# Kernel tuning notes

Measured on AMD Instinct MI355X. Metric: run time of the kernel, lower is better.

The kernel has to match this reference:

```python
import jax, jax.numpy as jnp
import numpy as np

NUM_EXPERTS = 8
TOP_K = 2
RANK = 16
LORA_ALPHA = 32
SCALING = LORA_ALPHA / RANK  # 2.0


def setup_inputs() -> dict:
    key = jax.random.key(0)
    ks = jax.random.split(key, 6)
    B, S, D_IN, D_OUT = 4, 2048, 4096, 4096
    x = jax.random.normal(ks[0], (B, S, D_IN), dtype=jnp.float32)
    W_base = jax.random.normal(ks[1], (D_OUT, D_IN), dtype=jnp.float32) * 0.02
    b_base = jax.random.normal(ks[2], (D_OUT,), dtype=jnp.float32) * 0.02
    W_router = jax.random.normal(ks[3], (NUM_EXPERTS, D_IN), dtype=jnp.float32) * 0.02
    A = jax.random.normal(ks[4], (NUM_EXPERTS, RANK, D_IN), dtype=jnp.float32) * 0.02
    Bm = jax.random.normal(ks[5], (D_OUT, RANK), dtype=jnp.float32) * 0.02
    Bm = jnp.broadcast_to(Bm, (NUM_EXPERTS, D_OUT, RANK)) * jnp.arange(1, NUM_EXPERTS + 1, dtype=jnp.float32)[:, None, None] * 0.2
    return {"x": x, "W_base": W_base, "b_base": b_base, "W_router": W_router, "A": A, "B": Bm}


def reference(x, W_base, b_base, W_router, A, B):
    bs, seq, d_in = x.shape
    T = bs * seq
    xf = x.reshape(T, d_in)  # flatten tokens, as in torch .view(-1, d_in)

    # base linear layer
    base = xf @ W_base.T + b_base  # [T, d_out]

    # local router: logits -> top-k -> softmax over selected weights
    logits = xf @ W_router.T                      # [T, E]
    rw, sel = jax.lax.top_k(logits, TOP_K)        # [T, K] each
    rw = jax.nn.softmax(rw, axis=-1)              # router_norm == 'softmax'

    # per-token per-expert combine weight (zero for unselected experts);
    # mathematically identical to gather-LoRA-scatter since top-k experts
    # per token are distinct.
    onehot = jax.nn.one_hot(sel, NUM_EXPERTS, dtype=rw.dtype)  # [T, K, E]
    w = jnp.einsum('tk,tke->te', rw, onehot)                   # [T, E]

    # LoRA: down-project to tiny rank, weight, then up-project; contract
    # expert+rank together to avoid a [T, E, d_out] intermediate.
    h = jnp.einsum('td,erd->ter', xf, A)          # [T, E, r] (small)
    lora = jnp.einsum('ter,te,eor->to', h, w, B) * SCALING  # [T, d_out]

    return (base + lora).reshape(bs, seq, -1)
```

## Files before the change

kernel.cpp:

```cpp
#include <hip/hip_runtime.h>
#include <hip/hip_bf16.h>
#include <stdint.h>

#define T_TOKENS 8192
#define DIN      4096
#define DOUT     4096
#define NE       8
#define RANK     16
#define KEXT     128
#define KTOT     4224
#define NT       66
#define SCALING  2.0f

typedef __attribute__((ext_vector_type(8))) short   short8;
typedef __attribute__((ext_vector_type(4))) float   float4v;

__device__ __forceinline__ unsigned short f2bf(float f) {
    union { float f; unsigned int u; } c; c.f = f;
    unsigned int u = c.u;
    u += 0x7FFFu + ((u >> 16) & 1u);
    return (unsigned short)(u >> 16);
}

#define GLD_LDS(g, l) __builtin_amdgcn_global_load_lds( \
    (const __attribute__((address_space(1))) void*)(g), \
    (__attribute__((address_space(3))) void*)(l), 16, 0, 0)

__global__ __launch_bounds__(256) void k_front(const float* __restrict__ x,
                                               const float* __restrict__ Wr,
                                               const float* __restrict__ Wb,
                                               const float* __restrict__ A,
                                               const float* __restrict__ Bm,
                                               unsigned short* __restrict__ xa,
                                               unsigned short* __restrict__ Wa,
                                               unsigned short* __restrict__ Acat,
                                               float* __restrict__ w8) {
    int b = blockIdx.x;
    int tid = threadIdx.x;

    if (b < 2048) {
        int l = tid & 63, w = tid >> 6;
        int t = b * 4 + w;
        const float4* x4 = (const float4*)x;
        const float4* Wr4 = (const float4*)Wr;
        unsigned short* xarow = xa + (size_t)t * KTOT;

        float racc[NE];
#pragma unroll
        for (int e = 0; e < NE; e++) racc[e] = 0.f;

#pragma unroll 4
        for (int ci = 0; ci < 16; ci++) {
            float4 xv = x4[(size_t)t * 1024 + ci * 64 + l];
            ushort4 p;
            p.x = f2bf(xv.x); p.y = f2bf(xv.y);
            p.z = f2bf(xv.z); p.w = f2bf(xv.w);
            *(ushort4*)(xarow + (ci * 64 + l) * 4) = p;
#pragma unroll
            for (int e = 0; e < NE; e++) {
                float4 wv = Wr4[e * 1024 + ci * 64 + l];
                racc[e] += xv.x * wv.x + xv.y * wv.y + xv.z * wv.z + xv.w * wv.w;
            }
        }
#pragma unroll
        for (int e = 0; e < NE; e++) {
            float v = racc[e];
#pragma unroll
            for (int off = 32; off > 0; off >>= 1) v += __shfl_xor(v, off);
            racc[e] = v;
        }
        if (l == 0) {
            int e0 = 0;
#pragma unroll
            for (int e = 1; e < NE; e++) if (racc[e] > racc[e0]) e0 = e;
            int e1 = -1;
#pragma unroll
            for (int e = 0; e < NE; e++)
                if (e != e0 && (e1 < 0 || racc[e] > racc[e1])) e1 = e;
            float a1 = __expf(racc[e1] - racc[e0]);
            float inv = 1.0f / (1.0f + a1);
            float* wrow = w8 + t * NE;
#pragma unroll
            for (int e = 0; e < NE; e++)
                wrow[e] = (e == e0) ? inv * SCALING : ((e == e1) ? a1 * inv * SCALING : 0.f);
        }
    } else if (b < 6144) {
        int base = (b - 2048) * 1024 + tid;
#pragma unroll
        for (int j = 0; j < 4; j++) {
            int idx = base + j * 256;
            float4 v = ((const float4*)Wb)[idx];
            int o  = idx >> 10;
            int kc = idx & 1023;
            ushort4 p;
            p.x = f2bf(v.x); p.y = f2bf(v.y); p.z = f2bf(v.z); p.w = f2bf(v.w);
            *(ushort4*)(Wa + (size_t)o * KTOT + kc * 4) = p;
        }
    } else {
        int idx = (b - 6144) * 256 + tid;
        if (idx < 131072) {
            float4 v = ((const float4*)A)[idx];
            ushort4 p;
            p.x = f2bf(v.x); p.y = f2bf(v.y); p.z = f2bf(v.z); p.w = f2bf(v.w);
            *(ushort4*)(Acat + (size_t)idx * 4) = p;
        } else {
            int j = idx - 131072;
            int o = j >> 5;
            int q = j & 31;
            int e = q >> 2;
            float4 v = ((const float4*)Bm)[(size_t)e * 16384 + o * 4 + (q & 3)];
            ushort4 p;
            p.x = f2bf(v.x); p.y = f2bf(v.y); p.z = f2bf(v.z); p.w = f2bf(v.w);
            *(ushort4*)(Wa + (size_t)o * KTOT + DIN + q * 4) = p;
        }
    }
}

#define STAGEH(kt, bb) do { \
    int k0_ = (kt) * 128; \
    _Pragma("unroll") \
    for (int it_ = 0; it_ < 2; it_++) { \
        int c_ = it_ * 256 + tid; \
        int row_ = c_ >> 4, s_ = c_ & 15; \
        int kc_ = s_ ^ (row_ & 15); \
        GLD_LDS(xa + (size_t)(m0 + row_) * KTOT + k0_ + kc_ * 8, lds_x + (bb) * 4096 + c_ * 8); \
    } \
    _Pragma("unroll") \
    for (int it_ = 0; it_ < 8; it_++) { \
        int c_ = it_ * 256 + tid; \
        int row_ = c_ >> 4, s_ = c_ & 15; \
        int kc_ = s_ ^ (row_ & 15); \
        GLD_LDS(Acat + (size_t)row_ * DIN + k0_ + kc_ * 8, lds_a + (bb) * 16384 + c_ * 8); \
    } \
} while (0)

__global__ __launch_bounds__(256) void k_h(unsigned short* __restrict__ xa,
                                           const unsigned short* __restrict__ Acat,
                                           const float* __restrict__ w8) {
    __shared__ unsigned short lds_x[2 * 32 * 128];
    __shared__ unsigned short lds_a[2 * 128 * 128];
    int m0  = blockIdx.x * 32;
    int tid = threadIdx.x;
    int l = tid & 63, w = tid >> 6;
    int quad = l >> 4, lr = l & 15;

    float4v acc[2][2] = {};

    STAGEH(0, 0);
    for (int kt = 0; kt < 32; ++kt) {
        int bb = kt & 1;
        if (kt + 1 < 32) {
            STAGEH(kt + 1, bb ^ 1);
            asm volatile("s_waitcnt vmcnt(10)" ::: "memory");
        } else {
            asm volatile("s_waitcnt vmcnt(0)" ::: "memory");
        }
        __syncthreads();
        const unsigned short* lx = lds_x + bb * 4096;
        const unsigned short* la = lds_a + bb * 16384;
#pragma unroll
        for (int kk = 0; kk < 4; kk++) {
            int kc = kk * 4 + quad;
            short8 a[2], bfr[2];
#pragma unroll
            for (int mi = 0; mi < 2; mi++) {
                int row = mi * 16 + lr;
                a[mi] = *(const short8*)&lx[row * 128 + ((kc ^ lr) * 8)];
            }
#pragma unroll
            for (int ni = 0; ni < 2; ni++) {
                int row = w * 32 + ni * 16 + lr;
                bfr[ni] = *(const short8*)&la[row * 128 + ((kc ^ lr) * 8)];
            }
#pragma unroll
            for (int mi = 0; mi < 2; mi++)
#pragma unroll
                for (int ni = 0; ni < 2; ni++)
                    acc[mi][ni] = __builtin_amdgcn_mfma_f32_16x16x32_bf16(a[mi], bfr[ni], acc[mi][ni], 0, 0, 0);
        }
        __syncthreads();
    }

#pragma unroll
    for (int mi = 0; mi < 2; mi++)
#pragma unroll
        for (int ni = 0; ni < 2; ni++) {
            int col = w * 32 + ni * 16 + lr;
            int e = col >> 4;
#pragma unroll
            for (int i = 0; i < 4; i++) {
                int t = m0 + mi * 16 + quad * 4 + i;
                float v = acc[mi][ni][i] * w8[t * NE + e];
                xa[(size_t)t * KTOT + DIN + col] = f2bf(v);
            }
        }
}

#define LOADA(dst, basep, mlo) { \
    _Pragma("unroll") for (int i_ = 0; i_ < 4; i_++) \
        dst[i_] = *(const short8*)((basep) + aoff + ((mlo) + i_) * 1024); }
#define LOADB(dst, basep) { \
    _Pragma("unroll") for (int i_ = 0; i_ < 4; i_++) \
        dst[i_] = *(const short8*)((basep) + boff + i_ * 1024); }
#define MFMA44(mlo) { \
    __builtin_amdgcn_s_setprio(1); \
    _Pragma("unroll") for (int i_ = 0; i_ < 4; i_++) \
    _Pragma("unroll") for (int j_ = 0; j_ < 4; j_++) \
        acc[(mlo) + i_][j_] = __builtin_amdgcn_mfma_f32_16x16x32_bf16(af[i_], bf[j_], acc[(mlo) + i_][j_], 0, 0, 0); \
    __builtin_amdgcn_s_setprio(0); }
#define STAGE(srcP, regbase, ts, kh, tb) do { \
    const unsigned short* s_ = (srcP) + (size_t)((ts) * 64 + (kh) * 32); \
    char* d_ = smem + (regbase) + (tb) * 32768 + (kh) * 16384 + tid16; \
    GLD_LDS(s_, d_); \
    GLD_LDS(s_ + (size_t)128 * KTOT, d_ + 8192); \
} while (0)
#define BAR() __builtin_amdgcn_s_barrier()
#define LGKM0() do { asm volatile("s_waitcnt lgkmcnt(0)" ::: "memory"); \
                     __builtin_amdgcn_sched_barrier(0); } while (0)

__global__ __launch_bounds__(512, 2) void k_main(const unsigned short* __restrict__ xa,
                                                 const unsigned short* __restrict__ Wa,
                                                 const float* __restrict__ bias,
                                                 float* __restrict__ out) {
    extern __shared__ char smem[];
    int tid = threadIdx.x;
    int l = tid & 63, w = tid >> 6;
    int lr = l & 15, quad = l >> 4;
    int wm = w >> 2, wn = w & 3;

    int bid = blockIdx.x;
    int xcd = bid & 7, idx = bid >> 3;
    int bm  = (xcd & 3) * 8 + (idx & 7);
    int bn  = (xcd >> 2) * 8 + (idx >> 3);

    int laneoff = (lr * 4 + (quad ^ ((lr >> 1) & 3))) * 16;
    int aoff = wm * 8192 + laneoff;
    int boff = wn * 4096 + laneoff;

    int srow  = w * 16 + ((tid >> 2) & 15);
    int skq   = (tid & 3) ^ ((tid >> 3) & 3);
    int tid16 = tid * 16;
    const unsigned short* srcA = xa + (size_t)(bm * 256 + srow) * KTOT + skq * 8;
    const unsigned short* srcB = Wa + (size_t)(bn * 256 + srow) * KTOT + skq * 8;

    float4v acc[8][4] = {};
    short8 af[4], bf[4];

    STAGE(srcA, 0,     0, 0, 0);
    STAGE(srcB, 65536, 0, 0, 0);
    STAGE(srcA, 0,     0, 1, 0);
    STAGE(srcB, 65536, 0, 1, 0);
    STAGE(srcA, 0,     1, 0, 1);
    STAGE(srcB, 65536, 1, 0, 1);
    asm volatile("s_waitcnt vmcnt(4)" ::: "memory");
    BAR();

    for (int t = 0; t < NT; ++t) {
        int buf  = t & 1, nbuf = buf ^ 1;
        int ts1  = (t + 1 < NT) ? t + 1 : NT - 1;
        int ts2  = (t + 2 < NT) ? t + 2 : NT - 1;
        const char* pa = smem + buf * 32768;
        const char* pb = smem + 65536 + buf * 32768;

        LOADA(af, pa, 0);
        LOADB(bf, pb);
        STAGE(srcA, 0, ts1, 1, nbuf);
        BAR(); LGKM0();
        MFMA44(0);
        BAR();

        LOADA(af, pa, 4);
        STAGE(srcB, 65536, ts1, 1, nbuf);
        BAR(); LGKM0();
        MFMA44(4);
        BAR();

        LOADA(af, pa + 16384, 0);
        LOADB(bf, pb + 16384);
        STAGE(srcA, 0, ts2, 0, buf);
        BAR(); LGKM0();
        MFMA44(0);
        BAR();

        LOADA(af, pa + 16384, 4);
        STAGE(srcB, 65536, ts2, 0, buf);
        asm volatile("s_waitcnt vmcnt(4)" ::: "memory");
        BAR(); LGKM0();
        MFMA44(4);
        BAR();
    }
    asm volatile("s_waitcnt vmcnt(0)" ::: "memory");

    int trow0 = bm * 256 + wm * 128;
    int ocol0 = bn * 256 + wn * 64;
#pragma unroll
    for (int ni = 0; ni < 4; ni++) {
        int o = ocol0 + ni * 16 + lr;
        float bb = bias[o];
#pragma unroll
        for (int mi = 0; mi < 8; mi++) {
#pragma unroll
            for (int i = 0; i < 4; i++) {
                int trow = trow0 + mi * 16 + quad * 4 + i;
                out[(size_t)trow * DOUT + o] = acc[mi][ni][i] + bb;
            }
        }
    }
}

extern "C" void kernel_launch(void* const* d_in, const int* in_sizes, int n_in,
                              void* d_out, int out_size, void* d_ws, size_t ws_size,
                              hipStream_t stream) {
    const float* x  = (const float*)d_in[0];
    const float* Wb = (const float*)d_in[1];
    const float* bb = (const float*)d_in[2];
    const float* Wr = (const float*)d_in[3];
    const float* A  = (const float*)d_in[4];
    const float* Bm = (const float*)d_in[5];
    float* out = (float*)d_out;

    char* ws = (char*)d_ws;
    unsigned short* xa   = (unsigned short*)(ws);
    unsigned short* Wa   = (unsigned short*)(ws + 69206016);
    unsigned short* Acat = (unsigned short*)(ws + 69206016 + 34603008);
    float*          w8   = (float*)(ws + 69206016 + 34603008 + 1048576);

    static bool attr_done = false;
    if (!attr_done) {
        hipFuncSetAttribute((const void*)k_main,
                            hipFuncAttributeMaxDynamicSharedMemorySize, 131072);
        attr_done = true;
    }

    k_front<<<dim3(7168),  dim3(256), 0, stream>>>(x, Wr, Wb, A, Bm, xa, Wa, Acat, w8);
    k_h    <<<dim3(256),   dim3(256), 0, stream>>>(xa, Acat, w8);
    k_main <<<dim3(512),   dim3(512), 131072, stream>>>(xa, Wa, bb, out);
}
```

Measured before the change: 590.0 us.

## Double-buffer LDS fragment registers to overlap ds_reads with MFMA

```diff
diff --git a/kernel.cpp b/kernel.cpp
--- a/kernel.cpp
+++ b/kernel.cpp
@@ -196,17 +196,17 @@
         }
 }
 
-#define LOADA(dst, basep, mlo) { \
+#define LOADA4(dst, basep, mlo) { \
     _Pragma("unroll") for (int i_ = 0; i_ < 4; i_++) \
         dst[i_] = *(const short8*)((basep) + aoff + ((mlo) + i_) * 1024); }
-#define LOADB(dst, basep) { \
+#define LOADB4(dst, basep) { \
     _Pragma("unroll") for (int i_ = 0; i_ < 4; i_++) \
         dst[i_] = *(const short8*)((basep) + boff + i_ * 1024); }
-#define MFMA44(mlo) { \
+#define MFMA44V(A_, B_, mlo) { \
     __builtin_amdgcn_s_setprio(1); \
     _Pragma("unroll") for (int i_ = 0; i_ < 4; i_++) \
     _Pragma("unroll") for (int j_ = 0; j_ < 4; j_++) \
-        acc[(mlo) + i_][j_] = __builtin_amdgcn_mfma_f32_16x16x32_bf16(af[i_], bf[j_], acc[(mlo) + i_][j_], 0, 0, 0); \
+        acc[(mlo) + i_][j_] = __builtin_amdgcn_mfma_f32_16x16x32_bf16(A_[i_], B_[j_], acc[(mlo) + i_][j_], 0, 0, 0); \
     __builtin_amdgcn_s_setprio(0); }
 #define STAGE(srcP, regbase, ts, kh, tb) do { \
     const unsigned short* s_ = (srcP) + (size_t)((ts) * 64 + (kh) * 32); \
@@ -215,8 +215,8 @@
     GLD_LDS(s_ + (size_t)128 * KTOT, d_ + 8192); \
 } while (0)
 #define BAR() __builtin_amdgcn_s_barrier()
-#define LGKM0() do { asm volatile("s_waitcnt lgkmcnt(0)" ::: "memory"); \
-                     __builtin_amdgcn_sched_barrier(0); } while (0)
+#define LGKMC(n) do { asm volatile("s_waitcnt lgkmcnt(" #n ")" ::: "memory"); \
+                      __builtin_amdgcn_sched_barrier(0); } while (0)
 
 __global__ __launch_bounds__(512, 2) void k_main(const unsigned short* __restrict__ xa,
                                                  const unsigned short* __restrict__ Wa,
@@ -244,7 +244,7 @@
     const unsigned short* srcB = Wa + (size_t)(bn * 256 + srow) * KTOT + skq * 8;
 
     float4v acc[8][4] = {};
-    short8 af[4], bf[4];
+    short8 afA[4], afB[4], bfA[4], bfB[4];
 
     STAGE(srcA, 0,     0, 0, 0);
     STAGE(srcB, 65536, 0, 0, 0);
@@ -254,42 +254,47 @@
     STAGE(srcB, 65536, 1, 0, 1);
     asm volatile("s_waitcnt vmcnt(4)" ::: "memory");
     BAR();
+    LOADA4(afA, smem, 0);
+    LOADB4(bfA, smem + 65536);
 
     for (int t = 0; t < NT; ++t) {
         int buf  = t & 1, nbuf = buf ^ 1;
         int ts1  = (t + 1 < NT) ? t + 1 : NT - 1;
         int ts2  = (t + 2 < NT) ? t + 2 : NT - 1;
-        const char* pa = smem + buf * 32768;
-        const char* pb = smem + 65536 + buf * 32768;
-
-        LOADA(af, pa, 0);
-        LOADB(bf, pb);
+        const char* pa  = smem + buf * 32768;
+        const char* pb  = smem + 65536 + buf * 32768;
+        const char* pan = smem + nbuf * 32768;
+        const char* pbn = smem + 65536 + nbuf * 32768;
+
+        LOADA4(afB, pa, 4);
         STAGE(srcA, 0, ts1, 1, nbuf);
-        BAR(); LGKM0();
-        MFMA44(0);
-        BAR();
-
-        LOADA(af, pa, 4);
+        BAR(); LGKMC(4);
+        MFMA44V(afA, bfA, 0);
+        BAR();
+
+        LOADA4(afA, pa + 16384, 0);
+        LOADB4(bfB, pb + 16384);
         STAGE(srcB, 65536, ts1, 1, nbuf);
-        BAR(); LGKM0();
-        MFMA44(4);
-        BAR();
-
-        LOADA(af, pa + 16384, 0);
-        LOADB(bf, pb + 16384);
+        BAR(); LGKMC(8);
+        MFMA44V(afB, bfA, 4);
+        BAR();
+
+        LOADA4(afB, pa + 16384, 4);
         STAGE(srcA, 0, ts2, 0, buf);
-        BAR(); LGKM0();
-        MFMA44(0);
-        BAR();
-
-        LOADA(af, pa + 16384, 4);
+        BAR(); LGKMC(4);
+        MFMA44V(afA, bfB, 0);
+        BAR();
+
         STAGE(srcB, 65536, ts2, 0, buf);
         asm volatile("s_waitcnt vmcnt(4)" ::: "memory");
-        BAR(); LGKM0();
-        MFMA44(4);
-        BAR();
-    }
-    asm volatile("s_waitcnt vmcnt(0)" ::: "memory");
+        BAR();
+        LOADA4(afA, pan, 0);
+        LOADB4(bfA, pbn);
+        LGKMC(8);
+        MFMA44V(afB, bfB, 4);
+        BAR();
+    }
+    asm volatile("s_waitcnt vmcnt(0) lgkmcnt(0)" ::: "memory");
 
     int trow0 = bm * 256 + wm * 128;
     int ocol0 = bn * 256 + wn * 64;
```

Result: no change. 584.3 us (-1.0%).
